# Kernel tuning notes

Hardware: AMD Instinct MI355X
Metric: run time of the kernel (lower is better)

The kernel has to match this reference:

```python
import jax, jax.numpy as jnp
import numpy as np

N = 100000
E = 1600000
G = 64  # number of graphs
EPS = 1e-5
NEG_SLOPE = 0.2


def _gat_conv(x, W, a_src, a_dst, b, src, dst, n, H, C):
    # x: [n, in]; W: [in, H*C]; a_src/a_dst: [H, C]; b: [H*C]
    h = (x @ W).reshape(n, H, C)                      # [n,H,C]
    al_s = jnp.sum(h * a_src, axis=-1)                # [n,H]
    al_d = jnp.sum(h * a_dst, axis=-1)                # [n,H]
    score = jax.nn.leaky_relu(al_s[src] + al_d[dst], NEG_SLOPE)  # [E,H]
    # segment softmax over incoming edges of each dst node
    m = jax.ops.segment_max(score, dst, num_segments=n)
    ex = jnp.exp(score - jax.lax.stop_gradient(m)[dst])
    den = jax.ops.segment_sum(ex, dst, num_segments=n)
    alpha = ex / den[dst]                             # [E,H]
    out = jax.ops.segment_sum(alpha[:, :, None] * h[src], dst, num_segments=n)
    return out.reshape(n, H * C) + b


def _bn_relu(x, gamma, beta):
    mu = jnp.mean(x, axis=0)
    var = jnp.var(x, axis=0)  # biased, matches torch BN normalization
    return jax.nn.relu((x - mu) * jax.lax.rsqrt(var + EPS) * gamma + beta)


def setup_inputs() -> dict:
    key = jax.random.key(0)
    ks = jax.random.split(key, 32)
    d = {}
    d['x'] = jax.random.normal(ks[0], (N, 3), dtype=jnp.float32)
    d['edge_index'] = jax.random.randint(ks[1], (2, E), 0, N, dtype=jnp.int64)
    d['batch'] = jnp.sort(jax.random.randint(ks[2], (N,), 0, G, dtype=jnp.int64))
    def p(k, shape):
        return jax.random.normal(k, shape, dtype=jnp.float32) * 0.1
    # conv1: 3 -> 16, heads=2
    d['W1'] = p(ks[3], (3, 32)); d['as1'] = p(ks[4], (2, 16)); d['ad1'] = p(ks[5], (2, 16)); d['b1'] = p(ks[6], (32,))
    d['g1'] = jnp.ones((32,), jnp.float32); d['be1'] = jnp.zeros((32,), jnp.float32)
    # conv2: 32 -> 32, heads=2
    d['W2'] = p(ks[7], (32, 64)); d['as2'] = p(ks[8], (2, 32)); d['ad2'] = p(ks[9], (2, 32)); d['b2'] = p(ks[10], (64,))
    d['g2'] = jnp.ones((64,), jnp.float32); d['be2'] = jnp.zeros((64,), jnp.float32)
    # conv3: 64 -> 64, heads=2
    d['W3'] = p(ks[11], (64, 128)); d['as3'] = p(ks[12], (2, 64)); d['ad3'] = p(ks[13], (2, 64)); d['b3'] = p(ks[14], (128,))
    d['g3'] = jnp.ones((128,), jnp.float32); d['be3'] = jnp.zeros((128,), jnp.float32)
    d['fcw'] = p(ks[15], (128, 10)); d['fcb'] = p(ks[16], (10,))
    return d


def reference(x, edge_index, batch, W1, as1, ad1, b1, g1, be1, W2, as2, ad2, b2, g2, be2, W3, as3, ad3, b3, g3, be3, fcw, fcb):
    n = x.shape[0]
    loops = jnp.arange(n, dtype=edge_index.dtype)  # PyG GATConv add_self_loops=True
    src = jnp.concatenate([edge_index[0], loops])
    dst = jnp.concatenate([edge_index[1], loops])
    h = _bn_relu(_gat_conv(x, W1, as1, ad1, b1, src, dst, n, 2, 16), g1, be1)
    h = _bn_relu(_gat_conv(h, W2, as2, ad2, b2, src, dst, n, 2, 32), g2, be2)
    h = _bn_relu(_gat_conv(h, W3, as3, ad3, b3, src, dst, n, 2, 64), g3, be3)
    pooled = jax.ops.segment_max(h, batch, num_segments=G)  # [G,128]
    return pooled @ fcw + fcb
```

## Files before the change

### kernel.cpp

```cpp
#include <hip/hip_runtime.h>
#include <cstddef>

constexpr int NN = 100000;
constexpr int NE = 1600000;
constexpr int TE = NE + NN;
constexpr int NG = 64;
constexpr float EPS = 1e-5f;
constexpr float NEG_SLOPE = 0.2f;
constexpr int NREP = 16;

constexpr int NBUCK = 256;
constexpr int DPB = 391;
constexpr int PHB = 256;
constexpr int CH = (TE + PHB - 1) / PHB;

__device__ __forceinline__ unsigned short f2bf(float f) {
    unsigned u = __float_as_uint(f);
    u += 0x7fffu + ((u >> 16) & 1u);
    return (unsigned short)(u >> 16);
}
__device__ __forceinline__ float bf2f(unsigned short s) {
    return __uint_as_float((unsigned)s << 16);
}
__device__ __forceinline__ float bflo(unsigned u) { return __uint_as_float(u << 16); }
__device__ __forceinline__ float bfhi(unsigned u) { return __uint_as_float(u & 0xffff0000u); }


__global__ void k_hist(const int* __restrict__ ei, int* __restrict__ hist) {
    __shared__ int hcnt[NBUCK];
    for (int i = threadIdx.x; i < NBUCK; i += 256) hcnt[i] = 0;
    __syncthreads();
    int k = blockIdx.x;
    int e0 = k * CH, e1 = min(e0 + CH, TE);
    for (int e = e0 + threadIdx.x; e < e1; e += 256) {
        int d = (e < NE) ? ei[NE + e] : (e - NE);
        atomicAdd(&hcnt[d / DPB], 1);
    }
    __syncthreads();
    for (int b = threadIdx.x; b < NBUCK; b += 256) hist[b * PHB + k] = hcnt[b];
}

__global__ void k_scanA(int* __restrict__ hist, int* __restrict__ bsum) {
    __shared__ int ls[PHB];
    int b = blockIdx.x, t = threadIdx.x;
    int v = hist[b * PHB + t];
    ls[t] = v;
    __syncthreads();
    for (int off = 1; off < PHB; off <<= 1) {
        int add = (t >= off) ? ls[t - off] : 0;
        __syncthreads();
        ls[t] += add;
        __syncthreads();
    }
    hist[b * PHB + t] = ls[t] - v;
    if (t == PHB - 1) bsum[b] = ls[t];
}

__global__ void k_scanB(const int* __restrict__ bsum, int* __restrict__ bbase,
                        int* __restrict__ rowptr) {
    __shared__ int ls[NBUCK];
    int t = threadIdx.x;
    int v = bsum[t];
    ls[t] = v;
    __syncthreads();
    for (int off = 1; off < NBUCK; off <<= 1) {
        int add = (t >= off) ? ls[t - off] : 0;
        __syncthreads();
        ls[t] += add;
        __syncthreads();
    }
    bbase[t] = ls[t] - v;
    if (t == NBUCK - 1) { bbase[NBUCK] = ls[t]; rowptr[NN] = ls[t]; }
}

__global__ void k_scatter(const int* __restrict__ ei, const int* __restrict__ hist,
                          const int* __restrict__ bbase, int* __restrict__ pairs) {
    __shared__ int cur[NBUCK];
    int k = blockIdx.x;
    for (int b = threadIdx.x; b < NBUCK; b += 256) cur[b] = bbase[b] + hist[b * PHB + k];
    __syncthreads();
    int e0 = k * CH, e1 = min(e0 + CH, TE);
    for (int e = e0 + threadIdx.x; e < e1; e += 256) {
        int s, d;
        if (e < NE) { s = ei[e]; d = ei[NE + e]; } else { s = e - NE; d = s; }
        int b = d / DPB, ld = d - b * DPB;
        int pos = atomicAdd(&cur[b], 1);
        pairs[pos] = (s << 9) | ld;
    }
}

__global__ void k_csr(const int* __restrict__ pairs, const int* __restrict__ bbase,
                      int* __restrict__ rowptr, int* __restrict__ colsrc) {
    __shared__ int deg[DPB];
    __shared__ int exc[DPB];
    __shared__ int sc[512];
    int b = blockIdx.x, t = threadIdx.x;
    int base = bbase[b], cnt = bbase[b + 1] - base;
    int d0 = b * DPB;
    int ndst = min(DPB, NN - d0);
    for (int i = t; i < DPB; i += 256) deg[i] = 0;
    __syncthreads();
    for (int i = t; i < cnt; i += 256) atomicAdd(&deg[pairs[base + i] & 511], 1);
    __syncthreads();
    sc[t] = (t < DPB) ? deg[t] : 0;
    sc[t + 256] = (t + 256 < DPB) ? deg[t + 256] : 0;
    __syncthreads();
    for (int off = 1; off < 512; off <<= 1) {
        int a0 = (t >= off) ? sc[t - off] : 0;
        int a1 = (t + 256 >= off) ? sc[t + 256 - off] : 0;
        __syncthreads();
        sc[t] += a0; sc[t + 256] += a1;
        __syncthreads();
    }
    if (t < DPB) exc[t] = sc[t] - deg[t];
    if (t + 256 < DPB) exc[t + 256] = sc[t + 256] - deg[t + 256];
    __syncthreads();
    for (int i = t; i < ndst; i += 256) rowptr[d0 + i] = base + exc[i];
    for (int i = t; i < DPB; i += 256) deg[i] = 0;
    __syncthreads();
    for (int i = t; i < cnt; i += 256) {
        int p = pairs[base + i];
        int ld = p & 511;
        int s = (unsigned)p >> 9;
        int pos = base + exc[ld] + atomicAdd(&deg[ld], 1);
        colsrc[pos] = s;
    }
}


template <int IN, int OUT, bool BN, int GRP>
__global__ void k_transform(const void* __restrict__ xv, const float* __restrict__ W,
                            const float* __restrict__ a_src, const float* __restrict__ a_dst,
                            const float* __restrict__ bnrep,
                            const float* __restrict__ gamma, const float* __restrict__ beta,
                            unsigned short* __restrict__ h, float* __restrict__ als,
                            float* __restrict__ ald, int n) {
    constexpr int C = OUT / 2;
    constexpr int TPN = OUT / 4;
    constexpr int NB = 256 / TPN;
    __shared__ float4 Ws4[IN * TPN];
    __shared__ float xs[NB * IN];
    __shared__ float sbn[BN ? 2 * IN : 1];

    if constexpr (BN) {
        if (threadIdx.x < IN) {
            int c = threadIdx.x;
            float s = 0.f, ss = 0.f;
#pragma unroll
            for (int r = 0; r < NREP; ++r) {
                s  += bnrep[r * 2 * IN + c];
                ss += bnrep[r * 2 * IN + IN + c];
            }
            float mu = s / n;
            float var = ss / n - mu * mu;
            float sca = gamma[c] * rsqrtf(var + EPS);
            sbn[c] = sca;
            sbn[IN + c] = beta[c] - mu * sca;
        }
    }
    float* Wsf = (float*)Ws4;
    for (int i = threadIdx.x; i < IN * OUT; i += 256) Wsf[i] = W[i];
    __syncthreads();

    int nl = threadIdx.x / TPN, q = threadIdx.x % TPN;
    int hd = (q >= TPN / 2);
    int cc = (q - hd * (TPN / 2)) * 4;
    float4 as4 = *(const float4*)&a_src[hd * C + cc];
    float4 ad4 = *(const float4*)&a_dst[hd * C + cc];

    for (int g = 0; g < GRP; ++g) {
        int node0 = (blockIdx.x * GRP + g) * NB;
        if (node0 >= n) break;
        if constexpr (BN) {
            const unsigned* xu = (const unsigned*)xv + (size_t)node0 * IN / 2;
            for (int i = threadIdx.x; i < NB * IN / 2; i += 256) {
                int e0 = 2 * i;
                int nn = node0 + e0 / IN;
                unsigned u = (nn < n) ? xu[i] : 0u;
                int c0 = e0 % IN;
                float v0 = bflo(u) * sbn[c0] + sbn[IN + c0];
                float v1 = bfhi(u) * sbn[c0 + 1] + sbn[IN + c0 + 1];
                xs[e0]     = v0 > 0.f ? v0 : 0.f;
                xs[e0 + 1] = v1 > 0.f ? v1 : 0.f;
            }
        } else {
            const float* x = (const float*)xv;
            for (int i = threadIdx.x; i < NB * IN; i += 256) {
                int nn = node0 + i / IN;
                xs[i] = (nn < n) ? x[(size_t)nn * IN + (i % IN)] : 0.f;
            }
        }
        __syncthreads();
        int node = node0 + nl;
        float4 acc = {0.f, 0.f, 0.f, 0.f};
#pragma unroll
        for (int i = 0; i < IN; ++i) {
            float xv2 = xs[nl * IN + i];
            float4 w = Ws4[i * TPN + q];
            acc.x += xv2 * w.x; acc.y += xv2 * w.y; acc.z += xv2 * w.z; acc.w += xv2 * w.w;
        }
        if (node < n) {
            uint2 pk;
            pk.x = (unsigned)f2bf(acc.x) | ((unsigned)f2bf(acc.y) << 16);
            pk.y = (unsigned)f2bf(acc.z) | ((unsigned)f2bf(acc.w) << 16);
            *(uint2*)&h[(size_t)node * OUT + q * 4] = pk;
        }
        float ps = acc.x * as4.x + acc.y * as4.y + acc.z * as4.z + acc.w * as4.w;
        float pd = acc.x * ad4.x + acc.y * ad4.y + acc.z * ad4.z + acc.w * ad4.w;
#pragma unroll
        for (int m = 1; m < TPN / 2; m <<= 1) {
            ps += __shfl_xor(ps, m, 64);
            pd += __shfl_xor(pd, m, 64);
        }
        if ((q & (TPN / 2 - 1)) == 0 && node < n) {
            als[node * 2 + hd] = ps;
            ald[node * 2 + hd] = pd;
        }
        __syncthreads();
    }
}


__device__ __forceinline__ float lrelu(float v) { return v > 0.f ? v : NEG_SLOPE * v; }

template <int OUT>
__global__ void k_aggregate(const int* __restrict__ rowptr, const int* __restrict__ colsrc,
                            const unsigned short* __restrict__ h, const float* __restrict__ als,
                            const float* __restrict__ ald, unsigned short* __restrict__ out,
                            float* __restrict__ bnrep) {
    constexpr int LPE = OUT / 8;
    constexpr int EPI2 = 32 / LPE;
    __shared__ float rowbuf[8][OUT];
    __shared__ float4 etab[4][64];
    int wv = threadIdx.x >> 6;
    int lane = threadIdx.x & 63;
    int hw = lane >> 5, hl = lane & 31;
    int base = ((int)blockIdx.x * 4 + wv) * 2;
    int wid = base + hw;
    bool valid = wid < NN;

    int start = 0, cnt = 0;
    float2 dv = make_float2(0.f, 0.f);
    if (valid) {
        start = rowptr[wid];
        cnt = rowptr[wid + 1] - start;
        dv = ((const float2*)ald)[wid];
    }
    int mc = max(cnt, __shfl_xor(cnt, 32, 64));

    if (mc <= 32) {
        int e = start + hl;
        bool act = valid && (hl < cnt);
        int s = act ? colsrc[e] : 0;
        float2 av = act ? ((const float2*)als)[s] : make_float2(0.f, 0.f);
        float t0 = act ? lrelu(av.x + dv.x) : -1e30f;
        float t1 = act ? lrelu(av.y + dv.y) : -1e30f;
        float m0 = t0, m1 = t1;
#pragma unroll
        for (int off = 16; off; off >>= 1) {
            m0 = fmaxf(m0, __shfl_xor(m0, off, 32));
            m1 = fmaxf(m1, __shfl_xor(m1, off, 32));
        }
        float w0 = act ? __expf(t0 - m0) : 0.f;
        float w1 = act ? __expf(t1 - m1) : 0.f;
        float den0 = w0, den1 = w1;
#pragma unroll
        for (int off = 16; off; off >>= 1) {
            den0 += __shfl_xor(den0, off, 32);
            den1 += __shfl_xor(den1, off, 32);
        }
        etab[wv][lane] = make_float4(__int_as_float(s), w0, w1, 0.f);
        int sub = hl / LPE, cl = hl % LPE;
        bool head1 = (cl >= LPE / 2);
        float acc[8];
#pragma unroll
        for (int k = 0; k < 8; ++k) acc[k] = 0.f;
        for (int j0 = 0; j0 < cnt; j0 += EPI2) {
            int jj = j0 + sub;
            if (jj < cnt) {
                float4 ed = etab[wv][hw * 32 + jj];
                int sj = __float_as_int(ed.x);
                float wsel = head1 ? ed.z : ed.y;
                uint4 hv = *(const uint4*)&h[(size_t)sj * OUT + cl * 8];
                acc[0] += wsel * bflo(hv.x); acc[1] += wsel * bfhi(hv.x);
                acc[2] += wsel * bflo(hv.y); acc[3] += wsel * bfhi(hv.y);
                acc[4] += wsel * bflo(hv.z); acc[5] += wsel * bfhi(hv.z);
                acc[6] += wsel * bflo(hv.w); acc[7] += wsel * bfhi(hv.w);
            }
        }
#pragma unroll
        for (int m = LPE; m < 32; m <<= 1) {
#pragma unroll
            for (int k = 0; k < 8; ++k) acc[k] += __shfl_xor(acc[k], m, 32);
        }
        float inv = 1.f / (head1 ? den1 : den0);
        if (valid && sub == 0) {
            float o[8];
#pragma unroll
            for (int k = 0; k < 8; ++k) o[k] = acc[k] * inv;
            uint4 pk;
            pk.x = (unsigned)f2bf(o[0]) | ((unsigned)f2bf(o[1]) << 16);
            pk.y = (unsigned)f2bf(o[2]) | ((unsigned)f2bf(o[3]) << 16);
            pk.z = (unsigned)f2bf(o[4]) | ((unsigned)f2bf(o[5]) << 16);
            pk.w = (unsigned)f2bf(o[6]) | ((unsigned)f2bf(o[7]) << 16);
            *(uint4*)&out[(size_t)wid * OUT + cl * 8] = pk;
            *(float4*)&rowbuf[wv * 2 + hw][cl * 8] = make_float4(o[0], o[1], o[2], o[3]);
            *(float4*)&rowbuf[wv * 2 + hw][cl * 8 + 4] = make_float4(o[4], o[5], o[6], o[7]);
        } else if (!valid) {
            for (int c = hl; c < OUT; c += 32) rowbuf[wv * 2 + hw][c] = 0.f;
        }
    } else {
        for (int i = 0; i < 2; ++i) {
            int w2 = base + i;
            int rb = wv * 2 + i;
            if (w2 >= NN) {
                for (int c = lane; c < OUT; c += 64) rowbuf[rb][c] = 0.f;
                continue;
            }
            int st = rowptr[w2], en = rowptr[w2 + 1];
            float2 dv2 = ((const float2*)ald)[w2];
            constexpr int C = OUT / 2;
            float m0 = -1e30f, m1 = -1e30f;
            for (int e = st + lane; e < en; e += 64) {
                int s = colsrc[e];
                float t0 = lrelu(als[s * 2 + 0] + dv2.x);
                float t1 = lrelu(als[s * 2 + 1] + dv2.y);
                m0 = fmaxf(m0, t0); m1 = fmaxf(m1, t1);
            }
#pragma unroll
            for (int off = 32; off; off >>= 1) {
                m0 = fmaxf(m0, __shfl_xor(m0, off, 64));
                m1 = fmaxf(m1, __shfl_xor(m1, off, 64));
            }
            float den0 = 0.f, den1 = 0.f;
            for (int e = st + lane; e < en; e += 64) {
                int s = colsrc[e];
                float t0 = lrelu(als[s * 2 + 0] + dv2.x);
                float t1 = lrelu(als[s * 2 + 1] + dv2.y);
                den0 += __expf(t0 - m0); den1 += __expf(t1 - m1);
            }
#pragma unroll
            for (int off = 32; off; off >>= 1) {
                den0 += __shfl_xor(den0, off, 64);
                den1 += __shfl_xor(den1, off, 64);
            }
            float inv0 = 1.f / den0, inv1 = 1.f / den1;
            if constexpr (OUT == 128) {
                float a0 = 0.f, a1 = 0.f;
                for (int e = st; e < en; ++e) {
                    int s = colsrc[e];
                    float t0 = lrelu(als[s * 2 + 0] + dv2.x);
                    float t1 = lrelu(als[s * 2 + 1] + dv2.y);
                    float w0 = __expf(t0 - m0) * inv0;
                    float w1 = __expf(t1 - m1) * inv1;
                    a0 += w0 * bf2f(h[(size_t)s * OUT + lane]);
                    a1 += w1 * bf2f(h[(size_t)s * OUT + 64 + lane]);
                }
                out[(size_t)w2 * OUT + lane] = f2bf(a0);
                out[(size_t)w2 * OUT + 64 + lane] = f2bf(a1);
                rowbuf[rb][lane] = a0;
                rowbuf[rb][64 + lane] = a1;
            } else {
                int c = lane;
                bool act2 = c < OUT;
                float a0 = 0.f;
                for (int e = st; e < en; ++e) {
                    int s = colsrc[e];
                    float t0 = lrelu(als[s * 2 + 0] + dv2.x);
                    float t1 = lrelu(als[s * 2 + 1] + dv2.y);
                    float w = (c < C) ? __expf(t0 - m0) * inv0 : __expf(t1 - m1) * inv1;
                    if (act2) a0 += w * bf2f(h[(size_t)s * OUT + c]);
                }
                if (act2) { out[(size_t)w2 * OUT + c] = f2bf(a0); rowbuf[rb][c] = a0; }
            }
        }
    }
    __syncthreads();
    float* dst = &bnrep[(blockIdx.x & (NREP - 1)) * 2 * OUT];
    for (int c = threadIdx.x; c < OUT; c += 256) {
        float s = 0.f, ss = 0.f;
#pragma unroll
        for (int r = 0; r < 8; ++r) {
            float v = rowbuf[r][c];
            s += v; ss += v * v;
        }
        atomicAdd(&dst[c], s);
        atomicAdd(&dst[OUT + c], ss);
    }
}


__global__ void k_pool(const unsigned short* __restrict__ h, const int* __restrict__ batch,
                       const float* __restrict__ bnrep, const float* __restrict__ gamma,
                       const float* __restrict__ beta, float* __restrict__ pooled, int n) {
    const int K = 32;
    int c = threadIdx.x;
    float s = 0.f, ss = 0.f;
#pragma unroll
    for (int r = 0; r < NREP; ++r) {
        s  += bnrep[r * 256 + c];
        ss += bnrep[r * 256 + 128 + c];
    }
    float mu = s / n;
    float var = ss / n - mu * mu;
    float scale = gamma[c] * rsqrtf(var + EPS);
    float shift = beta[c] - mu * scale;
    int n0 = blockIdx.x * K;
    if (n0 >= n) return;
    int nend = min(n, n0 + K);
    int curg = batch[n0];
    float m = 0.f;
    for (int nn = n0; nn < nend; ++nn) {
        int g = batch[nn];
        if (g != curg) {
            atomicMax((int*)&pooled[curg * 128 + c], __float_as_int(m));
            m = 0.f; curg = g;
        }
        float v = bf2f(h[(size_t)nn * 128 + c]) * scale + shift;
        m = fmaxf(m, v > 0.f ? v : 0.f);
    }
    atomicMax((int*)&pooled[curg * 128 + c], __float_as_int(m));
}

__global__ void k_fc(const float* __restrict__ pooled, const float* __restrict__ fcw,
                     const float* __restrict__ fcb, float* __restrict__ out) {
    int t = threadIdx.x;
    if (t >= NG * 10) return;
    int g = t / 10, j = t % 10;
    float acc = fcb[j];
#pragma unroll
    for (int c = 0; c < 128; ++c) acc += pooled[g * 128 + c] * fcw[c * 10 + j];
    out[g * 10 + j] = acc;
}


extern "C" void kernel_launch(void* const* d_in, const int* in_sizes, int n_in,
                              void* d_out, int out_size, void* d_ws, size_t ws_size,
                              hipStream_t stream) {
    const float* x   = (const float*)d_in[0];
    const int*   ei  = (const int*)d_in[1];
    const int*   bat = (const int*)d_in[2];
    const float* W1  = (const float*)d_in[3];
    const float* as1 = (const float*)d_in[4];
    const float* ad1 = (const float*)d_in[5];
    const float* g1  = (const float*)d_in[7];
    const float* be1 = (const float*)d_in[8];
    const float* W2  = (const float*)d_in[9];
    const float* as2 = (const float*)d_in[10];
    const float* ad2 = (const float*)d_in[11];
    const float* g2  = (const float*)d_in[13];
    const float* be2 = (const float*)d_in[14];
    const float* W3  = (const float*)d_in[15];
    const float* as3 = (const float*)d_in[16];
    const float* ad3 = (const float*)d_in[17];
    const float* g3  = (const float*)d_in[19];
    const float* be3 = (const float*)d_in[20];
    const float* fcw = (const float*)d_in[21];
    const float* fcb = (const float*)d_in[22];
    float* out = (float*)d_out;

    char* w = (char*)d_ws;
    size_t off = 0;
    auto take = [&](size_t bytes) {
        void* p = w + off;
        off += (bytes + 255) & ~(size_t)255;
        return p;
    };
    constexpr size_t ZN = (size_t)NREP * 2 * (32 + 64 + 128) + NG * 128;
    char* zreg = (char*)take(ZN * 4);
    float* bnr1   = (float*)zreg;
    float* bnr2   = bnr1 + NREP * 64;
    float* bnr3   = bnr2 + NREP * 128;
    float* pooled = bnr3 + NREP * 256;

    int*   hist    = (int*)take((size_t)NBUCK * PHB * 4);
    int*   bsum    = (int*)take(NBUCK * 4);
    int*   bbase   = (int*)take((NBUCK + 1) * 4);
    int*   rowptr  = (int*)take((size_t)(NN + 1) * 4);
    int*   pairs   = (int*)take((size_t)TE * 4);
    int*   colsrc  = (int*)take((size_t)TE * 4);
    float* al_s    = (float*)take((size_t)NN * 2 * 4);
    float* al_d    = (float*)take((size_t)NN * 2 * 4);
    unsigned short* h0 = (unsigned short*)take((size_t)NN * 128 * 2);
    unsigned short* h1 = (unsigned short*)take((size_t)NN * 128 * 2);

    hipMemsetAsync(zreg, 0, ZN * 4, stream);

    k_hist<<<PHB, 256, 0, stream>>>(ei, hist);
    k_scanA<<<NBUCK, PHB, 0, stream>>>(hist, bsum);
    k_scanB<<<1, NBUCK, 0, stream>>>(bsum, bbase, rowptr);
    k_scatter<<<PHB, 256, 0, stream>>>(ei, hist, bbase, pairs);
    k_csr<<<NBUCK, 256, 0, stream>>>(pairs, bbase, rowptr, colsrc);

    const int AGG_BLOCKS = (NN + 7) / 8;

    k_transform<3, 32, false, 1><<<(NN + 31) / 32, 256, 0, stream>>>(
        x, W1, as1, ad1, nullptr, nullptr, nullptr, h0, al_s, al_d, NN);
    k_aggregate<32><<<AGG_BLOCKS, 256, 0, stream>>>(rowptr, colsrc, h0, al_s, al_d, h1, bnr1);

    k_transform<32, 64, true, 4><<<(NN + 63) / 64, 256, 0, stream>>>(
        h1, W2, as2, ad2, bnr1, g1, be1, h0, al_s, al_d, NN);
    k_aggregate<64><<<AGG_BLOCKS, 256, 0, stream>>>(rowptr, colsrc, h0, al_s, al_d, h1, bnr2);

    k_transform<64, 128, true, 4><<<(NN + 31) / 32, 256, 0, stream>>>(
        h1, W3, as3, ad3, bnr2, g2, be2, h0, al_s, al_d, NN);
    k_aggregate<128><<<AGG_BLOCKS, 256, 0, stream>>>(rowptr, colsrc, h0, al_s, al_d, h1, bnr3);

    k_pool<<<(NN + 31) / 32, 128, 0, stream>>>(h1, bat, bnr3, g3, be3, pooled, NN);
    k_fc<<<1, 640, 0, stream>>>(pooled, fcw, fcb, out);
}
```

Before: 366.3 us.

## Split aggregation into alpha and sliced gather kernels with column-sliced feature layout

Stores node features in 16-column slices (slice-major) so each gather block touches only one 32-byte slice per source node, aiming to improve cache locality for the random gathers. Softmax attention weights are precomputed once per layer into an edge-sized alpha buffer by a separate kernel, and a new gather kernel processes one slice per block with 16 edges in parallel per node. This adds an extra kernel launch per layer and about 13.6 MB of alpha writes and rereads, and the alpha and colsrc arrays are read again for every slice.

```diff
diff --git a/kernel.cpp b/kernel.cpp
--- a/kernel.cpp
+++ b/kernel.cpp
@@ -172,16 +172,18 @@
         int node0 = (blockIdx.x * GRP + g) * NB;
         if (node0 >= n) break;
         if constexpr (BN) {
-            const unsigned* xu = (const unsigned*)xv + (size_t)node0 * IN / 2;
+            const unsigned* xu = (const unsigned*)xv;
             for (int i = threadIdx.x; i < NB * IN / 2; i += 256) {
-                int e0 = 2 * i;
-                int nn = node0 + e0 / IN;
-                unsigned u = (nn < n) ? xu[i] : 0u;
-                int c0 = e0 % IN;
+                int s = i / (NB * 8);
+                int r = i % (NB * 8);
+                int node = r >> 3, pr = r & 7;
+                int nn = node0 + node;
+                unsigned u = (nn < n) ? xu[(size_t)s * NN * 8 + (size_t)nn * 8 + pr] : 0u;
+                int c0 = s * 16 + pr * 2;
                 float v0 = bflo(u) * sbn[c0] + sbn[IN + c0];
                 float v1 = bfhi(u) * sbn[c0 + 1] + sbn[IN + c0 + 1];
-                xs[e0]     = v0 > 0.f ? v0 : 0.f;
-                xs[e0 + 1] = v1 > 0.f ? v1 : 0.f;
+                xs[node * IN + c0]     = v0 > 0.f ? v0 : 0.f;
+                xs[node * IN + c0 + 1] = v1 > 0.f ? v1 : 0.f;
             }
         } else {
             const float* x = (const float*)xv;
@@ -203,7 +205,7 @@
             uint2 pk;
             pk.x = (unsigned)f2bf(acc.x) | ((unsigned)f2bf(acc.y) << 16);
             pk.y = (unsigned)f2bf(acc.z) | ((unsigned)f2bf(acc.w) << 16);
-            *(uint2*)&h[(size_t)node * OUT + q * 4] = pk;
+            *(uint2*)&h[(size_t)(q >> 2) * NN * 16 + (size_t)node * 16 + (q & 3) * 4] = pk;
         }
         float ps = acc.x * as4.x + acc.y * as4.y + acc.z * as4.z + acc.w * as4.w;
         float pd = acc.x * ad4.x + acc.y * ad4.y + acc.z * ad4.z + acc.w * ad4.w;
@@ -223,22 +225,15 @@
 
 __device__ __forceinline__ float lrelu(float v) { return v > 0.f ? v : NEG_SLOPE * v; }
 
-template <int OUT>
-__global__ void k_aggregate(const int* __restrict__ rowptr, const int* __restrict__ colsrc,
-                            const unsigned short* __restrict__ h, const float* __restrict__ als,
-                            const float* __restrict__ ald, unsigned short* __restrict__ out,
-                            float* __restrict__ bnrep) {
-    constexpr int LPE = OUT / 8;
-    constexpr int EPI2 = 32 / LPE;
-    __shared__ float rowbuf[8][OUT];
-    __shared__ float4 etab[4][64];
+__global__ void k_alpha(const int* __restrict__ rowptr, const int* __restrict__ colsrc,
+                        const float* __restrict__ als, const float* __restrict__ ald,
+                        float* __restrict__ alpha) {
     int wv = threadIdx.x >> 6;
     int lane = threadIdx.x & 63;
     int hw = lane >> 5, hl = lane & 31;
     int base = ((int)blockIdx.x * 4 + wv) * 2;
     int wid = base + hw;
     bool valid = wid < NN;
-
     int start = 0, cnt = 0;
     float2 dv = make_float2(0.f, 0.f);
     if (valid) {
@@ -269,57 +264,16 @@
             den0 += __shfl_xor(den0, off, 32);
             den1 += __shfl_xor(den1, off, 32);
         }
-        etab[wv][lane] = make_float4(__int_as_float(s), w0, w1, 0.f);
-        int sub = hl / LPE, cl = hl % LPE;
-        bool head1 = (cl >= LPE / 2);
-        float acc[8];
-#pragma unroll
-        for (int k = 0; k < 8; ++k) acc[k] = 0.f;
-        for (int j0 = 0; j0 < cnt; j0 += EPI2) {
-            int jj = j0 + sub;
-            if (jj < cnt) {
-                float4 ed = etab[wv][hw * 32 + jj];
-                int sj = __float_as_int(ed.x);
-                float wsel = head1 ? ed.z : ed.y;
-                uint4 hv = *(const uint4*)&h[(size_t)sj * OUT + cl * 8];
-                acc[0] += wsel * bflo(hv.x); acc[1] += wsel * bfhi(hv.x);
-                acc[2] += wsel * bflo(hv.y); acc[3] += wsel * bfhi(hv.y);
-                acc[4] += wsel * bflo(hv.z); acc[5] += wsel * bfhi(hv.z);
-                acc[6] += wsel * bflo(hv.w); acc[7] += wsel * bfhi(hv.w);
-            }
-        }
-#pragma unroll
-        for (int m = LPE; m < 32; m <<= 1) {
-#pragma unroll
-            for (int k = 0; k < 8; ++k) acc[k] += __shfl_xor(acc[k], m, 32);
-        }
-        float inv = 1.f / (head1 ? den1 : den0);
-        if (valid && sub == 0) {
-            float o[8];
-#pragma unroll
-            for (int k = 0; k < 8; ++k) o[k] = acc[k] * inv;
-            uint4 pk;
-            pk.x = (unsigned)f2bf(o[0]) | ((unsigned)f2bf(o[1]) << 16);
-            pk.y = (unsigned)f2bf(o[2]) | ((unsigned)f2bf(o[3]) << 16);
-            pk.z = (unsigned)f2bf(o[4]) | ((unsigned)f2bf(o[5]) << 16);
-            pk.w = (unsigned)f2bf(o[6]) | ((unsigned)f2bf(o[7]) << 16);
-            *(uint4*)&out[(size_t)wid * OUT + cl * 8] = pk;
-            *(float4*)&rowbuf[wv * 2 + hw][cl * 8] = make_float4(o[0], o[1], o[2], o[3]);
-            *(float4*)&rowbuf[wv * 2 + hw][cl * 8 + 4] = make_float4(o[4], o[5], o[6], o[7]);
-        } else if (!valid) {
-            for (int c = hl; c < OUT; c += 32) rowbuf[wv * 2 + hw][c] = 0.f;
+        if (act) {
+            alpha[e] = w0 / den0;
+            alpha[TE + e] = w1 / den1;
         }
     } else {
         for (int i = 0; i < 2; ++i) {
             int w2 = base + i;
-            int rb = wv * 2 + i;
-            if (w2 >= NN) {
-                for (int c = lane; c < OUT; c += 64) rowbuf[rb][c] = 0.f;
-                continue;
-            }
+            if (w2 >= NN) continue;
             int st = rowptr[w2], en = rowptr[w2 + 1];
             float2 dv2 = ((const float2*)ald)[w2];
-            constexpr int C = OUT / 2;
             float m0 = -1e30f, m1 = -1e30f;
             for (int e = st + lane; e < en; e += 64) {
                 int s = colsrc[e];
@@ -335,9 +289,8 @@
             float den0 = 0.f, den1 = 0.f;
             for (int e = st + lane; e < en; e += 64) {
                 int s = colsrc[e];
-                float t0 = lrelu(als[s * 2 + 0] + dv2.x);
-                float t1 = lrelu(als[s * 2 + 1] + dv2.y);
-                den0 += __expf(t0 - m0); den1 += __expf(t1 - m1);
+                den0 += __expf(lrelu(als[s * 2 + 0] + dv2.x) - m0);
+                den1 += __expf(lrelu(als[s * 2 + 1] + dv2.y) - m1);
             }
 #pragma unroll
             for (int off = 32; off; off >>= 1) {
@@ -345,47 +298,82 @@
                 den1 += __shfl_xor(den1, off, 64);
             }
             float inv0 = 1.f / den0, inv1 = 1.f / den1;
-            if constexpr (OUT == 128) {
-                float a0 = 0.f, a1 = 0.f;
-                for (int e = st; e < en; ++e) {
-                    int s = colsrc[e];
-                    float t0 = lrelu(als[s * 2 + 0] + dv2.x);
-                    float t1 = lrelu(als[s * 2 + 1] + dv2.y);
-                    float w0 = __expf(t0 - m0) * inv0;
-                    float w1 = __expf(t1 - m1) * inv1;
-                    a0 += w0 * bf2f(h[(size_t)s * OUT + lane]);
-                    a1 += w1 * bf2f(h[(size_t)s * OUT + 64 + lane]);
-                }
-                out[(size_t)w2 * OUT + lane] = f2bf(a0);
-                out[(size_t)w2 * OUT + 64 + lane] = f2bf(a1);
-                rowbuf[rb][lane] = a0;
-                rowbuf[rb][64 + lane] = a1;
-            } else {
-                int c = lane;
-                bool act2 = c < OUT;
-                float a0 = 0.f;
-                for (int e = st; e < en; ++e) {
-                    int s = colsrc[e];
-                    float t0 = lrelu(als[s * 2 + 0] + dv2.x);
-                    float t1 = lrelu(als[s * 2 + 1] + dv2.y);
-                    float w = (c < C) ? __expf(t0 - m0) * inv0 : __expf(t1 - m1) * inv1;
-                    if (act2) a0 += w * bf2f(h[(size_t)s * OUT + c]);
-                }
-                if (act2) { out[(size_t)w2 * OUT + c] = f2bf(a0); rowbuf[rb][c] = a0; }
-            }
-        }
-    }
-    __syncthreads();
-    float* dst = &bnrep[(blockIdx.x & (NREP - 1)) * 2 * OUT];
-    for (int c = threadIdx.x; c < OUT; c += 256) {
+            for (int e = st + lane; e < en; e += 64) {
+                int s = colsrc[e];
+                alpha[e] = __expf(lrelu(als[s * 2 + 0] + dv2.x) - m0) * inv0;
+                alpha[TE + e] = __expf(lrelu(als[s * 2 + 1] + dv2.y) - m1) * inv1;
+            }
+        }
+    }
+}
+
+
+template <int OUT>
+__global__ void k_gather(const int* __restrict__ rowptr, const int* __restrict__ colsrc,
+                         const unsigned short* __restrict__ h, const float* __restrict__ alpha,
+                         unsigned short* __restrict__ out, float* __restrict__ bnrep) {
+    constexpr int NSLICE = OUT / 16;
+    __shared__ float rowbuf[8][16];
+    int slice = blockIdx.x % NSLICE;
+    int chunk = blockIdx.x / NSLICE;
+    int head = (slice * 32) / OUT;
+    const unsigned short* hsl = h + (size_t)slice * NN * 16;
+    unsigned short* osl = out + (size_t)slice * NN * 16;
+    const float* al = alpha + (size_t)head * TE;
+    int wv = threadIdx.x >> 6, lane = threadIdx.x & 63;
+    int hw = lane >> 5, hl = lane & 31;
+    int hwIdx = wv * 2 + hw;
+    int node = chunk * 8 + hwIdx;
+    int j = hl & 15, p = hl >> 4;
+    float acc[8];
+#pragma unroll
+    for (int k = 0; k < 8; ++k) acc[k] = 0.f;
+
+    if (node < NN) {
+        int start = rowptr[node], cnt = rowptr[node + 1] - start;
+        for (int j0 = 0; j0 < cnt; j0 += 16) {
+            int jj = j0 + j;
+            if (jj < cnt) {
+                int e = start + jj;
+                int s = colsrc[e];
+                float a = al[e];
+                uint4 hv = *(const uint4*)&hsl[(size_t)s * 16 + p * 8];
+                acc[0] += a * bflo(hv.x); acc[1] += a * bfhi(hv.x);
+                acc[2] += a * bflo(hv.y); acc[3] += a * bfhi(hv.y);
+                acc[4] += a * bflo(hv.z); acc[5] += a * bfhi(hv.z);
+                acc[6] += a * bflo(hv.w); acc[7] += a * bfhi(hv.w);
+            }
+        }
+#pragma unroll
+        for (int m = 1; m < 16; m <<= 1) {
+#pragma unroll
+            for (int k = 0; k < 8; ++k) acc[k] += __shfl_xor(acc[k], m, 64);
+        }
+        if (j == 0) {
+            uint4 pk;
+            pk.x = (unsigned)f2bf(acc[0]) | ((unsigned)f2bf(acc[1]) << 16);
+            pk.y = (unsigned)f2bf(acc[2]) | ((unsigned)f2bf(acc[3]) << 16);
+            pk.z = (unsigned)f2bf(acc[4]) | ((unsigned)f2bf(acc[5]) << 16);
+            pk.w = (unsigned)f2bf(acc[6]) | ((unsigned)f2bf(acc[7]) << 16);
+            *(uint4*)&osl[(size_t)node * 16 + p * 8] = pk;
+#pragma unroll
+            for (int k = 0; k < 8; ++k) rowbuf[hwIdx][p * 8 + k] = acc[k];
+        }
+    } else if (j == 0) {
+#pragma unroll
+        for (int k = 0; k < 8; ++k) rowbuf[hwIdx][p * 8 + k] = 0.f;
+    }
+    __syncthreads();
+    if (threadIdx.x < 16) {
         float s = 0.f, ss = 0.f;
 #pragma unroll
         for (int r = 0; r < 8; ++r) {
-            float v = rowbuf[r][c];
+            float v = rowbuf[r][threadIdx.x];
             s += v; ss += v * v;
         }
-        atomicAdd(&dst[c], s);
-        atomicAdd(&dst[OUT + c], ss);
+        float* dst = &bnrep[(chunk & (NREP - 1)) * 2 * OUT];
+        atomicAdd(&dst[slice * 16 + threadIdx.x], s);
+        atomicAdd(&dst[OUT + slice * 16 + threadIdx.x], ss);
     }
 }
 
@@ -405,6 +393,7 @@
     float var = ss / n - mu * mu;
     float scale = gamma[c] * rsqrtf(var + EPS);
     float shift = beta[c] - mu * scale;
+    const unsigned short* hc = h + (size_t)(c >> 4) * NN * 16 + (c & 15);
     int n0 = blockIdx.x * K;
     if (n0 >= n) return;
     int nend = min(n, n0 + K);
@@ -416,7 +405,7 @@
             atomicMax((int*)&pooled[curg * 128 + c], __float_as_int(m));
             m = 0.f; curg = g;
         }
-        float v = bf2f(h[(size_t)nn * 128 + c]) * scale + shift;
+        float v = bf2f(hc[(size_t)nn * 16]) * scale + shift;
         m = fmaxf(m, v > 0.f ? v : 0.f);
     }
     atomicMax((int*)&pooled[curg * 128 + c], __float_as_int(m));
@@ -481,6 +470,7 @@
     int*   colsrc  = (int*)take((size_t)TE * 4);
     float* al_s    = (float*)take((size_t)NN * 2 * 4);
     float* al_d    = (float*)take((size_t)NN * 2 * 4);
+    float* alpha   = (float*)take((size_t)2 * TE * 4);
     unsigned short* h0 = (unsigned short*)take((size_t)NN * 128 * 2);
     unsigned short* h1 = (unsigned short*)take((size_t)NN * 128 * 2);
 
@@ -492,19 +482,23 @@
     k_scatter<<<PHB, 256, 0, stream>>>(ei, hist, bbase, pairs);
     k_csr<<<NBUCK, 256, 0, stream>>>(pairs, bbase, rowptr, colsrc);
 
-    const int AGG_BLOCKS = (NN + 7) / 8;
+    const int ALPHA_BLOCKS = (NN + 7) / 8;
+    const int NCHUNK = (NN + 7) / 8;
 
     k_transform<3, 32, false, 1><<<(NN + 31) / 32, 256, 0, stream>>>(
         x, W1, as1, ad1, nullptr, nullptr, nullptr, h0, al_s, al_d, NN);
-    k_aggregate<32><<<AGG_BLOCKS, 256, 0, stream>>>(rowptr, colsrc, h0, al_s, al_d, h1, bnr1);
+    k_alpha<<<ALPHA_BLOCKS, 256, 0, stream>>>(rowptr, colsrc, al_s, al_d, alpha);
+    k_gather<32><<<NCHUNK * 2, 256, 0, stream>>>(rowptr, colsrc, h0, alpha, h1, bnr1);
 
     k_transform<32, 64, true, 4><<<(NN + 63) / 64, 256, 0, stream>>>(
         h1, W2, as2, ad2, bnr1, g1, be1, h0, al_s, al_d, NN);
-    k_aggregate<64><<<AGG_BLOCKS, 256, 0, stream>>>(rowptr, colsrc, h0, al_s, al_d, h1, bnr2);
+    k_alpha<<<ALPHA_BLOCKS, 256, 0, stream>>>(rowptr, colsrc, al_s, al_d, alpha);
+    k_gather<64><<<NCHUNK * 4, 256, 0, stream>>>(rowptr, colsrc, h0, alpha, h1, bnr2);
 
     k_transform<64, 128, true, 4><<<(NN + 31) / 32, 256, 0, stream>>>(
         h1, W3, as3, ad3, bnr2, g2, be2, h0, al_s, al_d, NN);
-    k_aggregate<128><<<AGG_BLOCKS, 256, 0, stream>>>(rowptr, colsrc, h0, al_s, al_d, h1, bnr3);
+    k_alpha<<<ALPHA_BLOCKS, 256, 0, stream>>>(rowptr, colsrc, al_s, al_d, alpha);
+    k_gather<128><<<NCHUNK * 8, 256, 0, stream>>>(rowptr, colsrc, h0, alpha, h1, bnr3);
 
     k_pool<<<(NN + 31) / 32, 128, 0, stream>>>(h1, bat, bnr3, g3, be3, pooled, NN);
     k_fc<<<1, 640, 0, stream>>>(pooled, fcw, fcb, out);
```

Result: slower. 493.4 us (+34.7%).
